# Kernel tuning notes

Measured on AMD Instinct MI355X. Metric: run time of the kernel, lower is better.

Reference implementation:

```python
import jax, jax.numpy as jnp
import numpy as np
import math

B, N = 64, 16384
POS_IN, HID, DIR_IN = 63, 128, 27
COLOR_IN = HID + DIR_IN  # 155
POS_W, POS_B = POS_IN * HID, HID          # 8064, 128
SIG_W, SIG_B = HID * 1, 1                  # 128, 1
COL_W, COL_B = COLOR_IN * 3, 3             # 465... actually 155*3=465? no: 465
TOTAL = POS_W + POS_B + SIG_W + SIG_B + COL_W + COL_B  # 8717


def pos_encode(x, num_freqs):
    # x: [..., 3] -> [..., 3 + 2*3*num_freqs], order: x, (sin f0, cos f0, sin f1, cos f1, ...)
    freqs = (2.0 ** jnp.arange(num_freqs, dtype=x.dtype)) * math.pi  # [L]
    xb = x[..., None, :] * freqs[:, None]                            # [..., L, 3]
    sc = jnp.stack([jnp.sin(xb), jnp.cos(xb)], axis=-2)              # [..., L, 2, 3]
    sc = sc.reshape(*x.shape[:-1], num_freqs * 2 * x.shape[-1])
    return jnp.concatenate([x, sc], axis=-1)


def setup_inputs() -> dict:
    key = jax.random.key(0)
    k1, k2, k3 = jax.random.split(key, 3)
    positions = jax.random.normal(k1, (B, N, 3), dtype=jnp.float32)
    directions = jax.random.normal(k2, (B, N, 3), dtype=jnp.float32)
    params = jax.random.normal(k3, (B, TOTAL), dtype=jnp.float32) * 0.1
    return {"positions": positions, "directions": directions, "params": params}


def reference(positions, directions, params):
    pos_enc = pos_encode(positions, 10)   # [B, N, 63]
    dir_enc = pos_encode(directions, 4)   # [B, N, 27]

    i = 0
    pw = params[:, i:i + POS_W].reshape(B, HID, POS_IN); i += POS_W
    pb = params[:, i:i + POS_B]; i += POS_B
    sw = params[:, i:i + SIG_W].reshape(B, 1, HID); i += SIG_W
    sb = params[:, i:i + SIG_B]; i += SIG_B
    cw = params[:, i:i + COL_W].reshape(B, 3, COLOR_IN); i += COL_W
    cb = params[:, i:i + COL_B]

    h = jnp.einsum('bnd,bhd->bnh', pos_enc, pw) + pb[:, None, :]
    h = jax.nn.relu(h)                                   # [B, N, 128]
    sigma = jnp.einsum('bnh,boh->bno', h, sw) + sb[:, None, :]  # [B, N, 1]
    h_dir = jnp.concatenate([h, dir_enc], axis=-1)       # [B, N, 155]
    rgb = jnp.einsum('bnc,boc->bno', h_dir, cw) + cb[:, None, :]
    rgb = jax.nn.sigmoid(rgb)                            # [B, N, 3]
    return sigma, rgb
```

## Files before the change

### kernel.cpp

```cpp
#include <hip/hip_runtime.h>
#include <hip/hip_bf16.h>


#define NB 64
#define NRAY 16384
#define NTOTAL 8789

typedef short bf16x8 __attribute__((ext_vector_type(8)));
typedef float f32x16 __attribute__((ext_vector_type(16)));

union U8 { unsigned u[4]; bf16x8 v; };

__device__ __forceinline__ unsigned pk2(float a, float b) {
    float2 t; t.x = a; t.y = b;
    __hip_bfloat162 h = __float22bfloat162_rn(t);
    return *reinterpret_cast<unsigned*>(&h);
}

#define MFMA __builtin_amdgcn_mfma_f32_32x32x16_bf16

__global__ __launch_bounds__(256, 3) void nerf_mfma_kernel(
    const float* __restrict__ pos,
    const float* __restrict__ dir,
    const float* __restrict__ params,
    float* __restrict__ out)
{
    const int tid  = threadIdx.x;
    const int lane = tid & 63;
    const int wid  = tid >> 6;
    const int hi   = lane >> 5;
    const int l31  = lane & 31;

    const int b   = blockIdx.x / 12;
    const int j   = blockIdx.x - b * 12;
    const int nit = (j < 4) ? 6 : 5;
    const int startChunk = (j < 4) ? j * 6 : 24 + (j - 4) * 5;
    const int chunk = startChunk << 8;
    const float* __restrict__ p = params + b * NTOTAL;

    __shared__ uint4 encs[2048];
    __shared__ uint4 awT[1024];
    __shared__ unsigned hawLds[256];
    char* encb = reinterpret_cast<char*>(encs);
    const char* awb  = reinterpret_cast<const char*>(awT);
    const char* hawb = reinterpret_cast<const char*>(hawLds);

    if (tid < 64) {
        const int s  = tid & 7;
        const int hh = (tid >> 3) & 1;
        const int r  = tid >> 4;
        const float* w2 = (r == 0) ? (p + 8192) : (p + 8321 + (r - 1) * 155);
        const int base = 32 * (s >> 1) + 16 * (s & 1) + 4 * hh;
        unsigned* dst = &hawLds[(((s << 1) + hh) * 4 + r) * 4];
        #pragma unroll
        for (int jj = 0; jj < 4; ++jj) {
            const int i0 = 2 * jj, i1 = 2 * jj + 1;
            dst[jj] = pk2(w2[base + (i0 & 3) + 8 * (i0 >> 2)],
                          w2[base + (i1 & 3) + 8 * (i1 >> 2)]);
        }
    }

    {
        const int h    = tid >> 1;
        const int half = tid & 1;
        const float* wrow = p + h * 63;
        const float bias  = p[8064 + h];
        char* dst = reinterpret_cast<char*>(awT) + h * 128;
        const int swz = (h & 7) << 4;
        #pragma unroll
        for (int c4 = 0; c4 < 4; ++c4) {
            const int c = half * 4 + c4;
            U8 u;
            #pragma unroll
            for (int jj = 0; jj < 4; ++jj) {
                const int k0 = 8 * c + 2 * jj, k1 = k0 + 1;
                const float e0 = (k0 < 3) ? wrow[k0] : (k0 == 3 ? bias : wrow[k0 - 1]);
                const float e1 = (k1 < 3) ? wrow[k1] : (k1 == 3 ? bias : wrow[k1 - 1]);
                u.u[jj] = pk2(e0, e1);
            }
            *reinterpret_cast<uint4*>(dst + ((c * 16) ^ swz)) =
                *reinterpret_cast<uint4*>(&u);
        }
    }

    f32x16 FZ;
    #pragma unroll
    for (int i = 0; i < 16; ++i) FZ[i] = 0.f;

    const float sb  = p[8320];
    const float cb0 = p[8786], cb1 = p[8787], cb2 = p[8788];
    const float* __restrict__ cwr  = p + 8321 + 128;
    const float* __restrict__ cwg  = p + 8321 + 155 + 128;
    const float* __restrict__ cwb2 = p + 8321 + 310 + 128;

    const int rayBlock = b * NRAY + chunk;
    float* __restrict__ rgbout = out + (long)NB * NRAY;
    const long pb0 = (long)(rayBlock + tid) * 3;
    const int hoff = hi * 64 + (l31 & 3) * 16;

    auto encode_row = [&](const float3 Pv) {
        const int swz = (tid & 7) << 4;
        char* myrow = encb + tid * 128;
        float s0 = __builtin_amdgcn_sinf(0.5f * Pv.x), c0 = __builtin_amdgcn_cosf(0.5f * Pv.x);
        float s1 = __builtin_amdgcn_sinf(0.5f * Pv.y), c1 = __builtin_amdgcn_cosf(0.5f * Pv.y);
        float s2 = __builtin_amdgcn_sinf(0.5f * Pv.z), c2 = __builtin_amdgcn_cosf(0.5f * Pv.z);
        unsigned wb[4];
        wb[0] = pk2(Pv.x, Pv.y);
        wb[1] = pk2(Pv.z, 1.0f);
        #pragma unroll
        for (int f = 0; f < 10; ++f) {
            const int w = 2 + 3 * f;
            wb[(w + 0) & 3] = pk2(s0, s1);
            if (((w + 0) & 3) == 3) {
                uint4 v; v.x = wb[0]; v.y = wb[1]; v.z = wb[2]; v.w = wb[3];
                *reinterpret_cast<uint4*>(myrow + ((((w + 0) >> 2) * 16) ^ swz)) = v;
            }
            wb[(w + 1) & 3] = pk2(s2, c0);
            if (((w + 1) & 3) == 3) {
                uint4 v; v.x = wb[0]; v.y = wb[1]; v.z = wb[2]; v.w = wb[3];
                *reinterpret_cast<uint4*>(myrow + ((((w + 1) >> 2) * 16) ^ swz)) = v;
            }
            wb[(w + 2) & 3] = pk2(c1, c2);
            if (((w + 2) & 3) == 3) {
                uint4 v; v.x = wb[0]; v.y = wb[1]; v.z = wb[2]; v.w = wb[3];
                *reinterpret_cast<uint4*>(myrow + ((((w + 2) >> 2) * 16) ^ swz)) = v;
            }
            if (f < 9) {
                float t;
                t = 2.f * s0 * c0; c0 = fmaf(-2.f * s0, s0, 1.f); s0 = t;
                t = 2.f * s1 * c1; c1 = fmaf(-2.f * s1, s1, 1.f); s1 = t;
                t = 2.f * s2 * c2; c2 = fmaf(-2.f * s2, s2, 1.f); s2 = t;
            }
        }
    };

    float3 Pc = *reinterpret_cast<const float3*>(pos + pb0);
    float3 Dc = *reinterpret_cast<const float3*>(dir + pb0);
    encode_row(Pc);
    float3 Pn = *reinterpret_cast<const float3*>(pos + pb0 + 768);
    float3 Dn = *reinterpret_cast<const float3*>(dir + pb0 + 768);
    __syncthreads();

    #pragma unroll 1
    for (int it = 0; it < nit; ++it) {
        const int ray = rayBlock + it * 256 + tid;

        bf16x8 be0[4], be1[4];
        {
            const int row0 = wid * 64 + l31;
            const int swz0 = (row0 & 7) << 4;
            const int row1 = row0 + 32;
            const int swz1 = (row1 & 7) << 4;
            #pragma unroll
            for (int ks = 0; ks < 4; ++ks) {
                be0[ks] = *reinterpret_cast<const bf16x8*>(
                    encb + row0 * 128 + ((ks * 32 + hi * 16) ^ swz0));
                be1[ks] = *reinterpret_cast<const bf16x8*>(
                    encb + row1 * 128 + ((ks * 32 + hi * 16) ^ swz1));
            }
        }

        if (it < nit - 1) encode_row(Pn);

        float crd = 0.f, cgd = 0.f, cbd = 0.f;
        {
            float s0 = __builtin_amdgcn_sinf(0.5f * Dc.x), c0 = __builtin_amdgcn_cosf(0.5f * Dc.x);
            float s1 = __builtin_amdgcn_sinf(0.5f * Dc.y), c1 = __builtin_amdgcn_cosf(0.5f * Dc.y);
            float s2 = __builtin_amdgcn_sinf(0.5f * Dc.z), c2 = __builtin_amdgcn_cosf(0.5f * Dc.z);
            crd = fmaf(Dc.x, cwr[0], crd);  cgd = fmaf(Dc.x, cwg[0], cgd);  cbd = fmaf(Dc.x, cwb2[0], cbd);
            crd = fmaf(Dc.y, cwr[1], crd);  cgd = fmaf(Dc.y, cwg[1], cgd);  cbd = fmaf(Dc.y, cwb2[1], cbd);
            crd = fmaf(Dc.z, cwr[2], crd);  cgd = fmaf(Dc.z, cwg[2], cgd);  cbd = fmaf(Dc.z, cwb2[2], cbd);
            #pragma unroll
            for (int f = 0; f < 4; ++f) {
                const int jj = 3 + 6 * f;
                crd = fmaf(s0, cwr[jj+0], crd); cgd = fmaf(s0, cwg[jj+0], cgd); cbd = fmaf(s0, cwb2[jj+0], cbd);
                crd = fmaf(s1, cwr[jj+1], crd); cgd = fmaf(s1, cwg[jj+1], cgd); cbd = fmaf(s1, cwb2[jj+1], cbd);
                crd = fmaf(s2, cwr[jj+2], crd); cgd = fmaf(s2, cwg[jj+2], cgd); cbd = fmaf(s2, cwb2[jj+2], cbd);
                crd = fmaf(c0, cwr[jj+3], crd); cgd = fmaf(c0, cwg[jj+3], cgd); cbd = fmaf(c0, cwb2[jj+3], cbd);
                crd = fmaf(c1, cwr[jj+4], crd); cgd = fmaf(c1, cwg[jj+4], cgd); cbd = fmaf(c1, cwb2[jj+4], cbd);
                crd = fmaf(c2, cwr[jj+5], crd); cgd = fmaf(c2, cwg[jj+5], cgd); cbd = fmaf(c2, cwb2[jj+5], cbd);
                if (f < 3) {
                    float t;
                    t = 2.f * s0 * c0; c0 = fmaf(-2.f * s0, s0, 1.f); s0 = t;
                    t = 2.f * s1 * c1; c1 = fmaf(-2.f * s1, s1, 1.f); s1 = t;
                    t = 2.f * s2 * c2; c2 = fmaf(-2.f * s2, s2, 1.f); s2 = t;
                }
            }
        }

        float3 Pn2, Dn2;
        if (it < nit - 2) {
            Pn2 = *reinterpret_cast<const float3*>(pos + pb0 + (it + 2) * 768);
            Dn2 = *reinterpret_cast<const float3*>(dir + pb0 + (it + 2) * 768);
        }

        __builtin_amdgcn_s_setprio(1);
        f32x16 hacc0 = FZ, hacc1 = FZ;
        #pragma unroll 1
        for (int mt = 0; mt < 4; ++mt) {
            const int arow = (mt << 5) + l31;
            const int aswz = (arow & 7) << 4;
            const char* abase = awb + arow * 128;
            const bf16x8 awf0 = *reinterpret_cast<const bf16x8*>(abase + ((0  + hi * 16) ^ aswz));
            const bf16x8 awf1 = *reinterpret_cast<const bf16x8*>(abase + ((32 + hi * 16) ^ aswz));
            const bf16x8 awf2 = *reinterpret_cast<const bf16x8*>(abase + ((64 + hi * 16) ^ aswz));
            const bf16x8 awf3 = *reinterpret_cast<const bf16x8*>(abase + ((96 + hi * 16) ^ aswz));

            f32x16 a0 = MFMA(awf0, be0[0], FZ, 0, 0, 0);
            f32x16 a1 = MFMA(awf0, be1[0], FZ, 0, 0, 0);
            a0 = MFMA(awf1, be0[1], a0, 0, 0, 0);
            a1 = MFMA(awf1, be1[1], a1, 0, 0, 0);
            a0 = MFMA(awf2, be0[2], a0, 0, 0, 0);
            a1 = MFMA(awf2, be1[2], a1, 0, 0, 0);
            a0 = MFMA(awf3, be0[3], a0, 0, 0, 0);
            a1 = MFMA(awf3, be1[3], a1, 0, 0, 0);

            #pragma unroll
            for (int t = 0; t < 2; ++t) {
                const int rb = t * 8;
                U8 u0, u1;
                #pragma unroll
                for (int jj = 0; jj < 4; ++jj) {
                    u0.u[jj] = pk2(fmaxf(a0[rb + 2 * jj], 0.f),
                                   fmaxf(a0[rb + 2 * jj + 1], 0.f));
                    u1.u[jj] = pk2(fmaxf(a1[rb + 2 * jj], 0.f),
                                   fmaxf(a1[rb + 2 * jj + 1], 0.f));
                }
                const bf16x8 hw = *reinterpret_cast<const bf16x8*>(
                    hawb + (2 * mt + t) * 128 + hoff);
                hacc0 = MFMA(hw, u0.v, hacc0, 0, 0, 0);
                hacc1 = MFMA(hw, u1.v, hacc1, 0, 0, 0);
            }
        }
        __builtin_amdgcn_s_setprio(0);

        const float hv0 = hi ? hacc1[0] : hacc0[0];
        const float hv1 = hi ? hacc1[1] : hacc0[1];
        const float hv2 = hi ? hacc1[2] : hacc0[2];
        const float hv3 = hi ? hacc1[3] : hacc0[3];

        const float sig = hv0 + sb;
        float cr  = hv1 + cb0 + crd;
        float cg  = hv2 + cb1 + cgd;
        float cbl = hv3 + cb2 + cbd;

        cr  = 1.0f / (1.0f + __expf(-cr));
        cg  = 1.0f / (1.0f + __expf(-cg));
        cbl = 1.0f / (1.0f + __expf(-cbl));

        out[ray] = sig;
        float3 rgbv; rgbv.x = cr; rgbv.y = cg; rgbv.z = cbl;
        *reinterpret_cast<float3*>(rgbout + (long)ray * 3) = rgbv;

        Pn = Pn2; Dc = Dn; Dn = Dn2;
    }
}

extern "C" void kernel_launch(void* const* d_in, const int* in_sizes, int n_in,
                              void* d_out, int out_size, void* d_ws, size_t ws_size,
                              hipStream_t stream) {
    const float* pos    = (const float*)d_in[0];
    const float* dirs   = (const float*)d_in[1];
    const float* params = (const float*)d_in[2];
    float* out = (float*)d_out;

    dim3 grid(768);
    dim3 block(256);
    nerf_mfma_kernel<<<grid, block, 0, stream>>>(pos, dirs, params, out);
}
```

Before: 46.53 us.

## Store LDS operands in MFMA fragment order and use uniform 4-iteration blocks

Replaces the row-major XOR-swizzled LDS layouts for encodings and first-layer weights with a layout that matches the MFMA fragments, so each lane reads consecutive 16-byte chunks at fixed offsets with no swizzle arithmetic. The grid also changes from 768 blocks with uneven 5 or 6 iterations to 1024 blocks of exactly 4 iterations each. This removes address computation and the load imbalance between blocks, but it means more blocks each pay the per-block weight-staging prologue, and the bank-conflict behaviour of the new layout differs from the swizzled one.

```diff
diff --git a/kernel.cpp b/kernel.cpp
--- a/kernel.cpp
+++ b/kernel.cpp
@@ -5,6 +5,7 @@
 #define NB 64
 #define NRAY 16384
 #define NTOTAL 8789
+#define NIT 4
 
 typedef short bf16x8 __attribute__((ext_vector_type(8)));
 typedef float f32x16 __attribute__((ext_vector_type(16)));
@@ -31,11 +32,8 @@
     const int hi   = lane >> 5;
     const int l31  = lane & 31;
 
-    const int b   = blockIdx.x / 12;
-    const int j   = blockIdx.x - b * 12;
-    const int nit = (j < 4) ? 6 : 5;
-    const int startChunk = (j < 4) ? j * 6 : 24 + (j - 4) * 5;
-    const int chunk = startChunk << 8;
+    const int b     = blockIdx.x >> 4;
+    const int chunk = (blockIdx.x & 15) << 10;
     const float* __restrict__ p = params + b * NTOTAL;
 
     __shared__ uint4 encs[2048];
@@ -61,25 +59,23 @@
     }
 
     {
-        const int h    = tid >> 1;
-        const int half = tid & 1;
-        const float* wrow = p + h * 63;
-        const float bias  = p[8064 + h];
-        char* dst = reinterpret_cast<char*>(awT) + h * 128;
-        const int swz = (h & 7) << 4;
+        const int mt = wid;
+        const int hrow = mt * 32 + l31;
+        const float* wrow = p + hrow * 63;
+        const float bias  = p[8064 + hrow];
+        char* dst = reinterpret_cast<char*>(awT) + mt * 4096 + lane * 16;
         #pragma unroll
-        for (int c4 = 0; c4 < 4; ++c4) {
-            const int c = half * 4 + c4;
+        for (int ks = 0; ks < 4; ++ks) {
             U8 u;
             #pragma unroll
             for (int jj = 0; jj < 4; ++jj) {
-                const int k0 = 8 * c + 2 * jj, k1 = k0 + 1;
+                const int k0 = ks * 16 + hi * 8 + 2 * jj;
+                const int k1 = k0 + 1;
                 const float e0 = (k0 < 3) ? wrow[k0] : (k0 == 3 ? bias : wrow[k0 - 1]);
                 const float e1 = (k1 < 3) ? wrow[k1] : (k1 == 3 ? bias : wrow[k1 - 1]);
                 u.u[jj] = pk2(e0, e1);
             }
-            *reinterpret_cast<uint4*>(dst + ((c * 16) ^ swz)) =
-                *reinterpret_cast<uint4*>(&u);
+            *reinterpret_cast<uint4*>(dst + ks * 1024) = *reinterpret_cast<uint4*>(&u);
         }
     }
 
@@ -99,8 +95,7 @@
     const int hoff = hi * 64 + (l31 & 3) * 16;
 
     auto encode_row = [&](const float3 Pv) {
-        const int swz = (tid & 7) << 4;
-        char* myrow = encb + tid * 128;
+        char* wbase = encb + ((tid >> 5) * 4) * 1024 + (tid & 31) * 16;
         float s0 = __builtin_amdgcn_sinf(0.5f * Pv.x), c0 = __builtin_amdgcn_cosf(0.5f * Pv.x);
         float s1 = __builtin_amdgcn_sinf(0.5f * Pv.y), c1 = __builtin_amdgcn_cosf(0.5f * Pv.y);
         float s2 = __builtin_amdgcn_sinf(0.5f * Pv.z), c2 = __builtin_amdgcn_cosf(0.5f * Pv.z);
@@ -110,20 +105,15 @@
         #pragma unroll
         for (int f = 0; f < 10; ++f) {
             const int w = 2 + 3 * f;
-            wb[(w + 0) & 3] = pk2(s0, s1);
-            if (((w + 0) & 3) == 3) {
-                uint4 v; v.x = wb[0]; v.y = wb[1]; v.z = wb[2]; v.w = wb[3];
-                *reinterpret_cast<uint4*>(myrow + ((((w + 0) >> 2) * 16) ^ swz)) = v;
-            }
-            wb[(w + 1) & 3] = pk2(s2, c0);
-            if (((w + 1) & 3) == 3) {
-                uint4 v; v.x = wb[0]; v.y = wb[1]; v.z = wb[2]; v.w = wb[3];
-                *reinterpret_cast<uint4*>(myrow + ((((w + 1) >> 2) * 16) ^ swz)) = v;
-            }
-            wb[(w + 2) & 3] = pk2(c1, c2);
-            if (((w + 2) & 3) == 3) {
-                uint4 v; v.x = wb[0]; v.y = wb[1]; v.z = wb[2]; v.w = wb[3];
-                *reinterpret_cast<uint4*>(myrow + ((((w + 2) >> 2) * 16) ^ swz)) = v;
+            #pragma unroll
+            for (int k = 0; k < 3; ++k) {
+                const int wk = w + k;
+                wb[wk & 3] = (k == 0) ? pk2(s0, s1) : (k == 1) ? pk2(s2, c0) : pk2(c1, c2);
+                if ((wk & 3) == 3) {
+                    const int g = wk >> 2;
+                    uint4 v; v.x = wb[0]; v.y = wb[1]; v.z = wb[2]; v.w = wb[3];
+                    *reinterpret_cast<uint4*>(wbase + (g >> 1) * 1024 + (g & 1) * 512) = v;
+                }
             }
             if (f < 9) {
                 float t;
@@ -142,25 +132,20 @@
     __syncthreads();
 
     #pragma unroll 1
-    for (int it = 0; it < nit; ++it) {
+    for (int it = 0; it < NIT; ++it) {
         const int ray = rayBlock + it * 256 + tid;
 
         bf16x8 be0[4], be1[4];
         {
-            const int row0 = wid * 64 + l31;
-            const int swz0 = (row0 & 7) << 4;
-            const int row1 = row0 + 32;
-            const int swz1 = (row1 & 7) << 4;
+            const char* ebase = encb + (wid * 8) * 1024 + lane * 16;
             #pragma unroll
             for (int ks = 0; ks < 4; ++ks) {
-                be0[ks] = *reinterpret_cast<const bf16x8*>(
-                    encb + row0 * 128 + ((ks * 32 + hi * 16) ^ swz0));
-                be1[ks] = *reinterpret_cast<const bf16x8*>(
-                    encb + row1 * 128 + ((ks * 32 + hi * 16) ^ swz1));
-            }
-        }
-
-        if (it < nit - 1) encode_row(Pn);
+                be0[ks] = *reinterpret_cast<const bf16x8*>(ebase + ks * 1024);
+                be1[ks] = *reinterpret_cast<const bf16x8*>(ebase + (4 + ks) * 1024);
+            }
+        }
+
+        if (it < NIT - 1) encode_row(Pn);
 
         float crd = 0.f, cgd = 0.f, cbd = 0.f;
         {
@@ -189,7 +174,7 @@
         }
 
         float3 Pn2, Dn2;
-        if (it < nit - 2) {
+        if (it < NIT - 2) {
             Pn2 = *reinterpret_cast<const float3*>(pos + pb0 + (it + 2) * 768);
             Dn2 = *reinterpret_cast<const float3*>(dir + pb0 + (it + 2) * 768);
         }
@@ -198,13 +183,11 @@
         f32x16 hacc0 = FZ, hacc1 = FZ;
         #pragma unroll 1
         for (int mt = 0; mt < 4; ++mt) {
-            const int arow = (mt << 5) + l31;
-            const int aswz = (arow & 7) << 4;
-            const char* abase = awb + arow * 128;
-            const bf16x8 awf0 = *reinterpret_cast<const bf16x8*>(abase + ((0  + hi * 16) ^ aswz));
-            const bf16x8 awf1 = *reinterpret_cast<const bf16x8*>(abase + ((32 + hi * 16) ^ aswz));
-            const bf16x8 awf2 = *reinterpret_cast<const bf16x8*>(abase + ((64 + hi * 16) ^ aswz));
-            const bf16x8 awf3 = *reinterpret_cast<const bf16x8*>(abase + ((96 + hi * 16) ^ aswz));
+            const char* abase = awb + mt * 4096 + lane * 16;
+            const bf16x8 awf0 = *reinterpret_cast<const bf16x8*>(abase);
+            const bf16x8 awf1 = *reinterpret_cast<const bf16x8*>(abase + 1024);
+            const bf16x8 awf2 = *reinterpret_cast<const bf16x8*>(abase + 2048);
+            const bf16x8 awf3 = *reinterpret_cast<const bf16x8*>(abase + 3072);
 
             f32x16 a0 = MFMA(awf0, be0[0], FZ, 0, 0, 0);
             f32x16 a1 = MFMA(awf0, be1[0], FZ, 0, 0, 0);
@@ -264,7 +247,7 @@
     const float* params = (const float*)d_in[2];
     float* out = (float*)d_out;
 
-    dim3 grid(768);
+    dim3 grid(1024);
     dim3 block(256);
     nerf_mfma_kernel<<<grid, block, 0, stream>>>(pos, dirs, params, out);
 }
```

Measured after the change: 44.81 us. 3.7% less time.
